# Kernel tuning notes

Hardware: AMD Instinct MI355X
Metric: run time of the kernel (lower is better)

Reference implementation:

```python
import jax, jax.numpy as jnp
import numpy as np

B, D_IN, D_OUT = 16384, 2048, 2048
BN_EPS = 1e-5


def setup_inputs() -> dict:
    key = jax.random.key(0)
    ks = jax.random.split(key, 6)
    return {
        "x": jax.random.normal(ks[0], (B, D_IN), dtype=jnp.float32),
        "base_weight": jax.random.normal(ks[1], (D_OUT, D_IN), dtype=jnp.float32) * 0.1,
        "bias": jnp.zeros((D_OUT,), dtype=jnp.float32),
        "center": jax.random.normal(ks[2], (D_IN,), dtype=jnp.float32),
        "sharpness": jnp.ones((D_IN,), dtype=jnp.float32),
        "gamma": jnp.ones((D_OUT,), dtype=jnp.float32),
        "beta": jnp.zeros((D_OUT,), dtype=jnp.float32),
        "top_k": 256,
    }


def reference(x, base_weight, bias, center, sharpness, gamma, beta, top_k):
    # fuzzy membership: sigmoid(sharpness * (x - center))  -> [B, D_in]
    mu = jax.nn.sigmoid(sharpness * (x - center))
    b, d = mu.shape

    # OWA weighted membership: keep top_k memberships, scaled by
    # normalized linspace(1.0, 0.1, top_k) weights; zeros elsewhere.
    order = jnp.argsort(-mu, axis=1)                       # descending sort indices
    sorted_vals = jnp.take_along_axis(mu, order, axis=1)
    w = jnp.linspace(1.0, 0.1, top_k, dtype=mu.dtype)
    w = w / w.sum()
    owa = jnp.zeros_like(mu).at[
        jnp.arange(b)[:, None], order[:, :top_k]
    ].set(w[None, :] * sorted_vals[:, :top_k])

    # per-sample scaled matmul: bmm(W * mu_exp, x) == (owa * x) @ W^T
    out = (owa * x) @ base_weight.T + bias                 # [B, D_out]
    out = jax.nn.relu(out)

    # BatchNorm1d in training mode: batch mean, biased variance
    mean = out.mean(axis=0)
    var = out.var(axis=0)
    y = (out - mean) * jax.lax.rsqrt(var + BN_EPS) * gamma + beta
    return (y, mu)
```

## Files before the change

### kernel.cpp

```cpp
#include <hip/hip_runtime.h>
#include <stdint.h>

#define NB 16384
#define DI 2048
#define DO 2048
#define KTOP 256
#define LIST_CAP 384
#define MT (NB / 256)

typedef __attribute__((ext_vector_type(4))) float f32x4;
typedef __attribute__((ext_vector_type(8))) short s16x8;
typedef __attribute__((ext_vector_type(8))) unsigned short u16x8;

#define OWA_C0 7.10227273e-3f
#define OWA_C1 2.50668449e-5f

__device__ __forceinline__ ushort f2bf(float f) {
  uint32_t u = __float_as_uint(f);
  uint32_t r = (u + 0x7FFFu + ((u >> 16) & 1u)) >> 16;
  return (ushort)r;
}

__device__ __forceinline__ void gld_lds16(const void* g, void* l) {
  __builtin_amdgcn_global_load_lds((__attribute__((address_space(1))) void*)g,
                                   (__attribute__((address_space(3))) void*)l,
                                   16, 0, 0);
}

__global__ __launch_bounds__(256) void k_cvt(const float* __restrict__ W,
                                             ushort* __restrict__ Wb) {
  size_t i = ((size_t)blockIdx.x * 256 + threadIdx.x) * 8;
  float4 a = *(const float4*)(W + i);
  float4 b = *(const float4*)(W + i + 4);
  u16x8 o;
  o[0] = f2bf(a.x); o[1] = f2bf(a.y); o[2] = f2bf(a.z); o[3] = f2bf(a.w);
  o[4] = f2bf(b.x); o[5] = f2bf(b.y); o[6] = f2bf(b.z); o[7] = f2bf(b.w);
  *(u16x8*)(Wb + i) = o;
}

__global__ __launch_bounds__(256) void k_topk(
    const float* __restrict__ x, const float* __restrict__ center,
    const float* __restrict__ sharp, float* __restrict__ mu_out,
    ushort* __restrict__ A) {
  __shared__ __align__(16) float w_lds[DI];
  __shared__ uint32_t histR[8 * 256];
  __shared__ uint64_t list[LIST_CAP];
  __shared__ uint32_t scal[4];

  const int t = threadIdx.x;
  const int lane = t & 63;
  const int wv = t >> 6;
  const int row = blockIdx.x;
  const int base = t * 8;

  const float* xr = x + (size_t)row * DI + base;
  float4 xa = *(const float4*)(xr);
  float4 xb = *(const float4*)(xr + 4);
  float4 ca = *(const float4*)(center + base);
  float4 cb = *(const float4*)(center + base + 4);
  float4 sa = *(const float4*)(sharp + base);
  float4 sb = *(const float4*)(sharp + base + 4);

  float xv[8] = {xa.x, xa.y, xa.z, xa.w, xb.x, xb.y, xb.z, xb.w};
  float cv[8] = {ca.x, ca.y, ca.z, ca.w, cb.x, cb.y, cb.z, cb.w};
  float sv[8] = {sa.x, sa.y, sa.z, sa.w, sb.x, sb.y, sb.z, sb.w};
  float muv[8];
  uint32_t bits[8];
#pragma unroll
  for (int e = 0; e < 8; ++e) {
    float s = sv[e] * (xv[e] - cv[e]);
    float m = 1.0f / (1.0f + __expf(-s));
    muv[e] = m;
    bits[e] = __float_as_uint(m);
  }
  if (mu_out) {
    float4 m0; m0.x = muv[0]; m0.y = muv[1]; m0.z = muv[2]; m0.w = muv[3];
    float4 m1; m1.x = muv[4]; m1.y = muv[5]; m1.z = muv[6]; m1.w = muv[7];
    *(float4*)(mu_out + (size_t)row * DI + base) = m0;
    *(float4*)(mu_out + (size_t)row * DI + base + 4) = m1;
  }
  float4 z4; z4.x = z4.y = z4.z = z4.w = 0.f;
  *(float4*)(w_lds + base) = z4;
  *(float4*)(w_lds + base + 4) = z4;

  uint32_t maskHi = 0, pfx = 0;
  uint32_t k_rem = KTOP;
  const uint32_t rep = (uint32_t)(t & 7) * 256u;
#pragma unroll 1
  for (int pass = 0; pass < 4; ++pass) {
    const int shift = 24 - pass * 8;
#pragma unroll
    for (int i = 0; i < 8; ++i) histR[t + 256 * i] = 0;
    __syncthreads();
#pragma unroll
    for (int e = 0; e < 8; ++e) {
      uint32_t bb = bits[e];
      if ((bb & maskHi) == pfx)
        atomicAdd(&histR[rep + ((bb >> shift) & 255u)], 1u);
    }
    __syncthreads();
    if (wv == 0) {
      uint32_t c0 = 0, c1 = 0, c2 = 0, c3 = 0;
#pragma unroll
      for (int r = 0; r < 8; ++r) {
        const uint32_t* h = &histR[r * 256 + lane * 4];
        c0 += h[0]; c1 += h[1]; c2 += h[2]; c3 += h[3];
      }
      uint32_t s3 = c3, s2 = c2 + s3, s1 = c1 + s2, s0 = c0 + s1;
      uint32_t Tl = s0, suf = s0;
#pragma unroll
      for (int off = 1; off < 64; off <<= 1) {
        uint32_t vsh = __shfl_down(suf, off);
        if (lane + off < 64) suf += vsh;
      }
      uint32_t above = suf - Tl;
      uint32_t SS[4] = {s0 + above, s1 + above, s2 + above, s3 + above};
      uint32_t cc[4] = {c0, c1, c2, c3};
#pragma unroll
      for (int j = 0; j < 4; ++j) {
        if (SS[j] >= k_rem && (SS[j] - cc[j]) < k_rem) {
          scal[0] = (uint32_t)(lane * 4 + j);
          scal[1] = SS[j] - cc[j];
        }
      }
    }
    __syncthreads();
    uint32_t v = scal[0], g = scal[1];
    pfx |= (v << shift);
    maskHi |= (0xFFu << shift);
    k_rem -= g;
  }
  const uint32_t tb = pfx;

  if (t == 0) scal[2] = 0;
  __syncthreads();
#pragma unroll
  for (int e = 0; e < 8; ++e) {
    if (bits[e] >= tb) {
      uint32_t pos = atomicAdd(&scal[2], 1u);
      if (pos < LIST_CAP)
        list[pos] = ((uint64_t)bits[e] << 32) |
                    (uint64_t)(uint32_t)(DI - 1 - (base + e));
    }
  }
  __syncthreads();
  int L = (int)scal[2];
  if (L > LIST_CAP) L = LIST_CAP;

  for (int sIdx = t; sIdx < L; sIdx += 256) {
    uint64_t key = list[sIdx];
    int rank = 0;
#pragma unroll 4
    for (int j = 0; j < L; ++j) rank += (int)(list[j] > key);
    if (rank < KTOP) {
      int idx = DI - 1 - (int)((uint32_t)key & 0xFFFFFFFFu);
      w_lds[idx] = OWA_C0 - OWA_C1 * (float)rank;
    }
  }
  __syncthreads();

  u16x8 ov;
#pragma unroll
  for (int e = 0; e < 8; ++e) ov[e] = f2bf(w_lds[base + e] * muv[e] * xv[e]);
  *(u16x8*)(A + (size_t)row * DI + base) = ov;
}

#define HALFS 8192

#define MFMA(a, b, c) __builtin_amdgcn_mfma_f32_16x16x32_bf16(a, b, c, 0, 0, 0)

#define STAGE_A(U, h)                                                       \
  do {                                                                      \
    ushort* sl = lA + (((((U) & 1) << 1) + (h)) * HALFS);                   \
    gld_lds16(pA0 + (size_t)((h) * 128) * DI + (size_t)(U) * 64, sl + d0);  \
    gld_lds16(pA0 + (size_t)((h) * 128 + 64) * DI + (size_t)(U) * 64,       \
              sl + d1);                                                     \
  } while (0)

#define STAGE_B(U, h)                                                       \
  do {                                                                      \
    ushort* sl = lB + (((((U) & 1) << 1) + (h)) * HALFS);                   \
    gld_lds16(pB0 + (size_t)((h) * 128) * DI + (size_t)(U) * 64, sl + d0);  \
    gld_lds16(pB0 + (size_t)((h) * 128 + 64) * DI + (size_t)(U) * 64,       \
              sl + d1);                                                     \
  } while (0)

#define RD_A(BUF, slotp, rowb)                                              \
  do {                                                                      \
    const ushort* rp_ = (slotp) + ((rowb) + fr) * 64;                       \
    BUF[0] = *(const s16x8*)(rp_ + c0);                                     \
    BUF[1] = *(const s16x8*)(rp_ + c1);                                     \
    BUF[2] = *(const s16x8*)(rp_ + 16 * 64 + c0);                           \
    BUF[3] = *(const s16x8*)(rp_ + 16 * 64 + c1);                           \
  } while (0)

#define RD_B(slotp)                                                         \
  do {                                                                      \
    _Pragma("unroll") for (int ni = 0; ni < 4; ++ni) {                      \
      breg[ni][0] = *(const s16x8*)((slotp) + ni * 1024 + boff + c0);       \
      breg[ni][1] = *(const s16x8*)((slotp) + ni * 1024 + boff + c1);       \
    }                                                                       \
  } while (0)

#define MFMA_PHASE(q, BUF)                                                  \
  do {                                                                      \
    __builtin_amdgcn_s_setprio(1);                                          \
    _Pragma("unroll") for (int ni = 0; ni < 4; ++ni) {                      \
      acc[2 * (q)][ni] = MFMA(BUF[0], breg[ni][0], acc[2 * (q)][ni]);       \
      acc[2 * (q)][ni] = MFMA(BUF[1], breg[ni][1], acc[2 * (q)][ni]);       \
      acc[2 * (q) + 1][ni] = MFMA(BUF[2], breg[ni][0], acc[2 * (q) + 1][ni]); \
      acc[2 * (q) + 1][ni] = MFMA(BUF[3], breg[ni][1], acc[2 * (q) + 1][ni]); \
    }                                                                       \
    __builtin_amdgcn_s_setprio(0);                                          \
  } while (0)

#define PHASE(q, RD_STMT, STAGE_STMT, BUF, POST_STMT, TAIL_STMT, LG)        \
  do {                                                                      \
    RD_STMT;                                                                \
    STAGE_STMT;                                                             \
    __builtin_amdgcn_s_barrier();                                           \
    asm volatile("s_waitcnt lgkmcnt(" LG ")" ::: "memory");                 \
    __builtin_amdgcn_sched_barrier(0);                                      \
    MFMA_PHASE(q, BUF);                                                     \
    POST_STMT;                                                              \
    TAIL_STMT;                                                              \
    __builtin_amdgcn_s_barrier();                                           \
  } while (0)

__global__ __launch_bounds__(512, 2) void k_gemm(
    const ushort* __restrict__ A, const ushort* __restrict__ Wb,
    const float* __restrict__ bias, float* __restrict__ outp,
    float* __restrict__ psum, float* __restrict__ psumsq) {
  __shared__ __align__(16) ushort lA[4 * HALFS];
  __shared__ __align__(16) ushort lB[4 * HALFS];

  const int t = threadIdx.x;
  const int lane = t & 63;
  const int wv = t >> 6;
  const int wm = wv >> 2;
  const int wn = wv & 3;
  const int wm32 = wm * 32;
  const int fr = lane & 15;
  const int kg = lane >> 4;
  const int s = fr & 7;

  int bid = blockIdx.x;
  int orig = (bid & 7) * 64 + (bid >> 3);
  const int nb = orig & 7;
  const int mb = orig >> 3;
  const int m0 = mb * 256;
  const int n0 = nb * 256;

  const int srow0 = t >> 3;
  const int scol = ((t & 7) ^ (srow0 & 7)) * 8;
  const ushort* pA0 = A + (size_t)(m0 + srow0) * DI + scol;
  const ushort* pB0 = Wb + (size_t)(n0 + srow0) * DI + scol;
  const int d0 = t * 8;
  const int d1 = (512 + t) * 8;

  f32x4 acc[8][4];
#pragma unroll
  for (int i = 0; i < 8; ++i)
#pragma unroll
    for (int j = 0; j < 4; ++j) acc[i][j] = (f32x4){0.f, 0.f, 0.f, 0.f};

  const int c0 = (kg ^ s) * 8;
  const int c1 = ((4 + kg) ^ s) * 8;
  const int boff = ((wn & 1) * 64 + fr) * 64;

  s16x8 breg[4][2];
  s16x8 bufA_[4], bufB_[4];

  STAGE_B(0, 0); STAGE_B(0, 1);
  STAGE_A(0, 0); STAGE_A(0, 1);
  STAGE_B(1, 0); STAGE_B(1, 1);
  asm volatile("s_waitcnt vmcnt(6)" ::: "memory");
  __builtin_amdgcn_s_barrier();
  RD_B(lB + (wn >> 1) * HALFS);
  RD_A(bufA_, lA, wm32);

#pragma unroll 1
  for (int T = 0; T < 31; ++T) {
    const ushort* lAcur = lA + ((T & 1) << 1) * HALFS;
    const ushort* lAnxt = lA + (((T + 1) & 1) << 1) * HALFS;
    const ushort* sBnxt = lB + ((((T + 1) & 1) << 1) + (wn >> 1)) * HALFS;

    PHASE(0, RD_A(bufB_, lAcur, 64 + wm32), STAGE_A(T + 1, 0), bufA_, ,
          asm volatile("s_waitcnt vmcnt(6)" ::: "memory"), "4");
    PHASE(1, RD_A(bufA_, lAcur + HALFS, wm32), STAGE_A(T + 1, 1), bufB_, , ,
          "4");
    PHASE(2, RD_A(bufB_, lAcur + HALFS, 64 + wm32),
          if (T < 30) STAGE_B(T + 2, 0), bufA_, ,
          if (T < 30) { asm volatile("s_waitcnt vmcnt(4)" ::: "memory"); }
          else { asm volatile("s_waitcnt vmcnt(2)" ::: "memory"); }, "4");
    PHASE(3, RD_A(bufA_, lAnxt, wm32), if (T < 30) STAGE_B(T + 2, 1), bufB_,
          RD_B(sBnxt), , "4");
  }
  {
    const ushort* lAcur = lA + 2 * HALFS;
    PHASE(0, RD_A(bufB_, lAcur, 64 + wm32), , bufA_, ,
          asm volatile("s_waitcnt vmcnt(0)" ::: "memory"), "4");
    PHASE(1, RD_A(bufA_, lAcur + HALFS, wm32), , bufB_, , , "4");
    PHASE(2, RD_A(bufB_, lAcur + HALFS, 64 + wm32), , bufA_, , , "4");
    PHASE(3, , , bufB_, , , "0");
  }

  __syncthreads();
  float* colsum = (float*)lA;
  float* colsq = colsum + 256;
  if (t < 256) { colsum[t] = 0.f; colsq[t] = 0.f; }
  __syncthreads();
#pragma unroll
  for (int ni = 0; ni < 4; ++ni) {
    const int n = n0 + wn * 64 + ni * 16 + fr;
    const float bv = bias[n];
    float cs = 0.f, cq = 0.f;
#pragma unroll
    for (int mi = 0; mi < 8; ++mi) {
      const int rowb = m0 + 64 * (mi >> 1) + wm32 + 16 * (mi & 1) + kg * 4;
      f32x4 v = acc[mi][ni];
#pragma unroll
      for (int r = 0; r < 4; ++r) {
        float zz = fmaxf(v[r] + bv, 0.f);
        outp[(size_t)(rowb + r) * DO + n] = zz;
        cs += zz;
        cq += zz * zz;
      }
    }
    cs += __shfl_xor(cs, 16); cq += __shfl_xor(cq, 16);
    cs += __shfl_xor(cs, 32); cq += __shfl_xor(cq, 32);
    if (kg == 0) {
      atomicAdd(&colsum[wn * 64 + ni * 16 + fr], cs);
      atomicAdd(&colsq[wn * 64 + ni * 16 + fr], cq);
    }
  }
  __syncthreads();
  if (t < 256) {
    psum[(size_t)mb * DO + n0 + t] = colsum[t];
    psumsq[(size_t)mb * DO + n0 + t] = colsq[t];
  }
}

__global__ __launch_bounds__(256) void k_bnfin(
    const float* __restrict__ psum, const float* __restrict__ psumsq,
    const float* __restrict__ gamma, const float* __restrict__ beta,
    float* __restrict__ scaleA, float* __restrict__ shiftA) {
  int n = blockIdx.x * 256 + threadIdx.x;
  float s = 0.f, q = 0.f;
  for (int r = 0; r < MT; ++r) {
    s += psum[(size_t)r * DO + n];
    q += psumsq[(size_t)r * DO + n];
  }
  float mean = s * (1.0f / (float)NB);
  float var = q * (1.0f / (float)NB) - mean * mean;
  var = fmaxf(var, 0.f);
  float rstd = rsqrtf(var + 1e-5f);
  float sc = gamma[n] * rstd;
  scaleA[n] = sc;
  shiftA[n] = beta[n] - mean * sc;
}

__global__ __launch_bounds__(256) void k_bnapply(float* __restrict__ outp,
                                                 const float* __restrict__ scaleA,
                                                 const float* __restrict__ shiftA) {
  size_t i = ((size_t)blockIdx.x * 256 + threadIdx.x) * 4;
  int n = (int)(i & (DO - 1));
  float4 v = *(float4*)(outp + i);
  float4 sc = *(const float4*)(scaleA + n);
  float4 sh = *(const float4*)(shiftA + n);
  v.x = v.x * sc.x + sh.x;
  v.y = v.y * sc.y + sh.y;
  v.z = v.z * sc.z + sh.z;
  v.w = v.w * sc.w + sh.w;
  *(float4*)(outp + i) = v;
}

__global__ __launch_bounds__(256) void k_mu(const float* __restrict__ x,
                                            const float* __restrict__ center,
                                            const float* __restrict__ sharp,
                                            float* __restrict__ mu_out) {
  const int t = threadIdx.x;
  const int row = blockIdx.x;
  const int base = t * 8;
  const float* xr = x + (size_t)row * DI + base;
  float4 xa = *(const float4*)(xr);
  float4 xb = *(const float4*)(xr + 4);
  float4 ca = *(const float4*)(center + base);
  float4 cb = *(const float4*)(center + base + 4);
  float4 sa = *(const float4*)(sharp + base);
  float4 sb = *(const float4*)(sharp + base + 4);
  float xv[8] = {xa.x, xa.y, xa.z, xa.w, xb.x, xb.y, xb.z, xb.w};
  float cv[8] = {ca.x, ca.y, ca.z, ca.w, cb.x, cb.y, cb.z, cb.w};
  float sv[8] = {sa.x, sa.y, sa.z, sa.w, sb.x, sb.y, sb.z, sb.w};
  float mu[8];
#pragma unroll
  for (int e = 0; e < 8; ++e) {
    float s = sv[e] * (xv[e] - cv[e]);
    mu[e] = 1.0f / (1.0f + __expf(-s));
  }
  float4 m0; m0.x = mu[0]; m0.y = mu[1]; m0.z = mu[2]; m0.w = mu[3];
  float4 m1; m1.x = mu[4]; m1.y = mu[5]; m1.z = mu[6]; m1.w = mu[7];
  *(float4*)(mu_out + (size_t)row * DI + base) = m0;
  *(float4*)(mu_out + (size_t)row * DI + base + 4) = m1;
}

extern "C" void kernel_launch(void* const* d_in, const int* in_sizes, int n_in,
                              void* d_out, int out_size, void* d_ws, size_t ws_size,
                              hipStream_t stream) {
  (void)in_sizes; (void)n_in; (void)out_size;
  const float* x = (const float*)d_in[0];
  const float* W = (const float*)d_in[1];
  const float* bias = (const float*)d_in[2];
  const float* center = (const float*)d_in[3];
  const float* sharp = (const float*)d_in[4];
  const float* gamma = (const float*)d_in[5];
  const float* beta = (const float*)d_in[6];

  float* outY = (float*)d_out;
  float* outMu = outY + (size_t)NB * DO;

  const size_t A_BYTES = (size_t)NB * DI * 2;
  const size_t WB_BYTES = (size_t)DO * DI * 2;
  const size_t PS_BYTES = (size_t)MT * DO * 4;
  const size_t SC_BYTES = (size_t)DO * 4;
  const size_t NEED_BIG = A_BYTES + WB_BYTES + 2 * PS_BYTES + 2 * SC_BYTES;

  char* p = (char*)d_ws;
  bool bigws = (ws_size >= NEED_BIG);
  ushort* A;
  if (bigws) { A = (ushort*)p; p += A_BYTES; }
  else       { A = (ushort*)outMu; }
  ushort* Wb = (ushort*)p; p += WB_BYTES;
  float* psum = (float*)p; p += PS_BYTES;
  float* psumsq = (float*)p; p += PS_BYTES;
  float* scaleA = (float*)p; p += SC_BYTES;
  float* shiftA = (float*)p;

  k_cvt<<<dim3((DO * DI) / (256 * 8)), dim3(256), 0, stream>>>(W, Wb);
  k_topk<<<dim3(NB), dim3(256), 0, stream>>>(x, center, sharp,
                                             bigws ? outMu : (float*)nullptr, A);
  k_gemm<<<dim3((NB / 256) * (DO / 256)), dim3(512), 0, stream>>>(A, Wb, bias, outY,
                                                                  psum, psumsq);
  k_bnfin<<<dim3(DO / 256), dim3(256), 0, stream>>>(psum, psumsq, gamma, beta,
                                                    scaleA, shiftA);
  k_bnapply<<<dim3((size_t)NB * DO / 4 / 256), dim3(256), 0, stream>>>(outY, scaleA,
                                                                       shiftA);
  if (!bigws) k_mu<<<dim3(NB), dim3(256), 0, stream>>>(x, center, sharp, outMu);
}
```

Before: 374.5 us.

## Process one row per wavefront in top-k kernel to remove block barriers

Result: slower. 413.7 us (+10.5%).

```diff
diff --git a/kernel.cpp b/kernel.cpp
--- a/kernel.cpp
+++ b/kernel.cpp
@@ -5,7 +5,7 @@
 #define DI 2048
 #define DO 2048
 #define KTOP 256
-#define LIST_CAP 384
+#define LCAP 320
 #define MT (NB / 256)
 
 typedef __attribute__((ext_vector_type(4))) float f32x4;
@@ -25,6 +25,11 @@
   __builtin_amdgcn_global_load_lds((__attribute__((address_space(1))) void*)g,
                                    (__attribute__((address_space(3))) void*)l,
                                    16, 0, 0);
+}
+
+__device__ __forceinline__ void WB() {
+  __builtin_amdgcn_wave_barrier();
+  __builtin_amdgcn_sched_barrier(0);
 }
 
 __global__ __launch_bounds__(256) void k_cvt(const float* __restrict__ W,
@@ -42,127 +47,151 @@
     const float* __restrict__ x, const float* __restrict__ center,
     const float* __restrict__ sharp, float* __restrict__ mu_out,
     ushort* __restrict__ A) {
-  __shared__ __align__(16) float w_lds[DI];
-  __shared__ uint32_t histR[8 * 256];
-  __shared__ uint64_t list[LIST_CAP];
-  __shared__ uint32_t scal[4];
-
-  const int t = threadIdx.x;
-  const int lane = t & 63;
-  const int wv = t >> 6;
-  const int row = blockIdx.x;
-  const int base = t * 8;
-
-  const float* xr = x + (size_t)row * DI + base;
-  float4 xa = *(const float4*)(xr);
-  float4 xb = *(const float4*)(xr + 4);
-  float4 ca = *(const float4*)(center + base);
-  float4 cb = *(const float4*)(center + base + 4);
-  float4 sa = *(const float4*)(sharp + base);
-  float4 sb = *(const float4*)(sharp + base + 4);
-
-  float xv[8] = {xa.x, xa.y, xa.z, xa.w, xb.x, xb.y, xb.z, xb.w};
-  float cv[8] = {ca.x, ca.y, ca.z, ca.w, cb.x, cb.y, cb.z, cb.w};
-  float sv[8] = {sa.x, sa.y, sa.z, sa.w, sb.x, sb.y, sb.z, sb.w};
-  float muv[8];
-  uint32_t bits[8];
-#pragma unroll
-  for (int e = 0; e < 8; ++e) {
-    float s = sv[e] * (xv[e] - cv[e]);
-    float m = 1.0f / (1.0f + __expf(-s));
-    muv[e] = m;
-    bits[e] = __float_as_uint(m);
-  }
-  if (mu_out) {
-    float4 m0; m0.x = muv[0]; m0.y = muv[1]; m0.z = muv[2]; m0.w = muv[3];
-    float4 m1; m1.x = muv[4]; m1.y = muv[5]; m1.z = muv[6]; m1.w = muv[7];
-    *(float4*)(mu_out + (size_t)row * DI + base) = m0;
-    *(float4*)(mu_out + (size_t)row * DI + base + 4) = m1;
-  }
-  float4 z4; z4.x = z4.y = z4.z = z4.w = 0.f;
-  *(float4*)(w_lds + base) = z4;
-  *(float4*)(w_lds + base + 4) = z4;
-
-  uint32_t maskHi = 0, pfx = 0;
-  uint32_t k_rem = KTOP;
-  const uint32_t rep = (uint32_t)(t & 7) * 256u;
+  __shared__ uint32_t hist[4][2][256];
+  __shared__ uint64_t lst[4][LCAP];
+  __shared__ ushort rnk[4][DI];
+  __shared__ uint32_t scal2[4][2];
+
+  const int lane = threadIdx.x & 63;
+  const int wv = threadIdx.x >> 6;
+  const int row = blockIdx.x * 4 + wv;
+  const int cb = lane * 32;
+
+  const float* xr = x + (size_t)row * DI + cb;
+  float p[32];
+  uint32_t bits[32];
+#pragma unroll
+  for (int c = 0; c < 8; ++c) {
+    float4 xv = *(const float4*)(xr + c * 4);
+    float4 cv = *(const float4*)(center + cb + c * 4);
+    float4 sv = *(const float4*)(sharp + cb + c * 4);
+    float m0 = 1.0f / (1.0f + __expf(-(sv.x * (xv.x - cv.x))));
+    float m1 = 1.0f / (1.0f + __expf(-(sv.y * (xv.y - cv.y))));
+    float m2 = 1.0f / (1.0f + __expf(-(sv.z * (xv.z - cv.z))));
+    float m3 = 1.0f / (1.0f + __expf(-(sv.w * (xv.w - cv.w))));
+    if (mu_out) {
+      float4 mo; mo.x = m0; mo.y = m1; mo.z = m2; mo.w = m3;
+      *(float4*)(mu_out + (size_t)row * DI + cb + c * 4) = mo;
+    }
+    bits[c * 4 + 0] = __float_as_uint(m0);
+    bits[c * 4 + 1] = __float_as_uint(m1);
+    bits[c * 4 + 2] = __float_as_uint(m2);
+    bits[c * 4 + 3] = __float_as_uint(m3);
+    p[c * 4 + 0] = m0 * xv.x;
+    p[c * 4 + 1] = m1 * xv.y;
+    p[c * 4 + 2] = m2 * xv.z;
+    p[c * 4 + 3] = m3 * xv.w;
+  }
+
+  {
+    uint32_t* hb = &hist[wv][0][0];
+    uint4 z; z.x = z.y = z.z = z.w = 0u;
+    *(uint4*)(hb + lane * 8) = z;
+    *(uint4*)(hb + lane * 8 + 4) = z;
+    uint4 ff; ff.x = ff.y = ff.z = ff.w = ~0u;
+    uint4* rb = (uint4*)&rnk[wv][0];
+    rb[lane * 4 + 0] = ff; rb[lane * 4 + 1] = ff;
+    rb[lane * 4 + 2] = ff; rb[lane * 4 + 3] = ff;
+  }
+  WB();
+
+  uint32_t maskHi = 0, pfx = 0, krem = KTOP;
+  uint32_t* h0 = &hist[wv][lane & 1][0];
 #pragma unroll 1
   for (int pass = 0; pass < 4; ++pass) {
     const int shift = 24 - pass * 8;
 #pragma unroll
-    for (int i = 0; i < 8; ++i) histR[t + 256 * i] = 0;
-    __syncthreads();
+    for (int c = 0; c < 32; ++c) {
+      if ((bits[c] & maskHi) == pfx)
+        atomicAdd(&h0[(bits[c] >> shift) & 255u], 1u);
+    }
+    WB();
+    uint4 ha = *(uint4*)&hist[wv][0][lane * 4];
+    uint4 hb4 = *(uint4*)&hist[wv][1][lane * 4];
+    uint32_t c0 = ha.x + hb4.x, c1 = ha.y + hb4.y;
+    uint32_t c2 = ha.z + hb4.z, c3 = ha.w + hb4.w;
+    uint32_t s3 = c3, s2 = c2 + s3, s1 = c1 + s2, s0 = c0 + s1;
+    uint32_t suf = s0;
+#pragma unroll
+    for (int off = 1; off < 64; off <<= 1) {
+      uint32_t v = __shfl_down(suf, off);
+      if (lane + off < 64) suf += v;
+    }
+    uint32_t above = suf - s0;
+    uint32_t SS0 = s0 + above, SS1 = s1 + above;
+    uint32_t SS2 = s2 + above, SS3 = s3 + above;
+    if (SS0 >= krem && SS0 - c0 < krem) { scal2[wv][0] = lane * 4 + 0; scal2[wv][1] = SS0 - c0; }
+    if (SS1 >= krem && SS1 - c1 < krem) { scal2[wv][0] = lane * 4 + 1; scal2[wv][1] = SS1 - c1; }
+    if (SS2 >= krem && SS2 - c2 < krem) { scal2[wv][0] = lane * 4 + 2; scal2[wv][1] = SS2 - c2; }
+    if (SS3 >= krem && SS3 - c3 < krem) { scal2[wv][0] = lane * 4 + 3; scal2[wv][1] = SS3 - c3; }
+    WB();
+    uint32_t d = scal2[wv][0], g = scal2[wv][1];
+    pfx |= (d << shift);
+    maskHi |= (0xFFu << shift);
+    krem -= g;
+    WB();
+    if (pass < 3) {
+      uint32_t* hb = &hist[wv][0][0];
+      uint4 z; z.x = z.y = z.z = z.w = 0u;
+      *(uint4*)(hb + lane * 8) = z;
+      *(uint4*)(hb + lane * 8 + 4) = z;
+      WB();
+    }
+  }
+  const uint32_t tb = pfx;
+
+  uint32_t Lc = 0;
+#pragma unroll
+  for (int c = 0; c < 32; ++c) {
+    bool pr = (bits[c] >= tb);
+    uint64_t m = __ballot(pr);
+    if (pr) {
+      uint32_t pos = Lc + (uint32_t)__popcll(m & ((1ull << lane) - 1ull));
+      if (pos < LCAP)
+        lst[wv][pos] = ((uint64_t)bits[c] << 32) |
+                       (uint64_t)(uint32_t)(DI - 1 - (cb + c));
+    }
+    Lc += (uint32_t)__popcll(m);
+  }
+  WB();
+  const int L = (Lc > LCAP) ? LCAP : (int)Lc;
+
+  uint64_t ck[5];
+#pragma unroll
+  for (int m2 = 0; m2 < 5; ++m2) {
+    int i2 = lane + 64 * m2;
+    ck[m2] = (i2 < L) ? lst[wv][i2] : ~0ull;
+  }
+  uint32_t rk[5] = {0, 0, 0, 0, 0};
+#pragma unroll 2
+  for (int j = 0; j < L; ++j) {
+    uint64_t kj = lst[wv][j];
+#pragma unroll
+    for (int m2 = 0; m2 < 5; ++m2) rk[m2] += (uint32_t)(kj > ck[m2]);
+  }
+  WB();
+#pragma unroll
+  for (int m2 = 0; m2 < 5; ++m2) {
+    int i2 = lane + 64 * m2;
+    if (i2 < L && rk[m2] < KTOP) {
+      int col = DI - 1 - (int)(uint32_t)(ck[m2] & 0xFFFFFFFFu);
+      rnk[wv][col] = (ushort)rk[m2];
+    }
+  }
+  WB();
+
+#pragma unroll
+  for (int g8 = 0; g8 < 4; ++g8) {
+    u16x8 rv = *(u16x8*)&rnk[wv][cb + g8 * 8];
+    u16x8 ov;
 #pragma unroll
     for (int e = 0; e < 8; ++e) {
-      uint32_t bb = bits[e];
-      if ((bb & maskHi) == pfx)
-        atomicAdd(&histR[rep + ((bb >> shift) & 255u)], 1u);
-    }
-    __syncthreads();
-    if (wv == 0) {
-      uint32_t c0 = 0, c1 = 0, c2 = 0, c3 = 0;
-#pragma unroll
-      for (int r = 0; r < 8; ++r) {
-        const uint32_t* h = &histR[r * 256 + lane * 4];
-        c0 += h[0]; c1 += h[1]; c2 += h[2]; c3 += h[3];
-      }
-      uint32_t s3 = c3, s2 = c2 + s3, s1 = c1 + s2, s0 = c0 + s1;
-      uint32_t Tl = s0, suf = s0;
-#pragma unroll
-      for (int off = 1; off < 64; off <<= 1) {
-        uint32_t vsh = __shfl_down(suf, off);
-        if (lane + off < 64) suf += vsh;
-      }
-      uint32_t above = suf - Tl;
-      uint32_t SS[4] = {s0 + above, s1 + above, s2 + above, s3 + above};
-      uint32_t cc[4] = {c0, c1, c2, c3};
-#pragma unroll
-      for (int j = 0; j < 4; ++j) {
-        if (SS[j] >= k_rem && (SS[j] - cc[j]) < k_rem) {
-          scal[0] = (uint32_t)(lane * 4 + j);
-          scal[1] = SS[j] - cc[j];
-        }
-      }
-    }
-    __syncthreads();
-    uint32_t v = scal[0], g = scal[1];
-    pfx |= (v << shift);
-    maskHi |= (0xFFu << shift);
-    k_rem -= g;
-  }
-  const uint32_t tb = pfx;
-
-  if (t == 0) scal[2] = 0;
-  __syncthreads();
-#pragma unroll
-  for (int e = 0; e < 8; ++e) {
-    if (bits[e] >= tb) {
-      uint32_t pos = atomicAdd(&scal[2], 1u);
-      if (pos < LIST_CAP)
-        list[pos] = ((uint64_t)bits[e] << 32) |
-                    (uint64_t)(uint32_t)(DI - 1 - (base + e));
-    }
-  }
-  __syncthreads();
-  int L = (int)scal[2];
-  if (L > LIST_CAP) L = LIST_CAP;
-
-  for (int sIdx = t; sIdx < L; sIdx += 256) {
-    uint64_t key = list[sIdx];
-    int rank = 0;
-#pragma unroll 4
-    for (int j = 0; j < L; ++j) rank += (int)(list[j] > key);
-    if (rank < KTOP) {
-      int idx = DI - 1 - (int)((uint32_t)key & 0xFFFFFFFFu);
-      w_lds[idx] = OWA_C0 - OWA_C1 * (float)rank;
-    }
-  }
-  __syncthreads();
-
-  u16x8 ov;
-#pragma unroll
-  for (int e = 0; e < 8; ++e) ov[e] = f2bf(w_lds[base + e] * muv[e] * xv[e]);
-  *(u16x8*)(A + (size_t)row * DI + base) = ov;
+      uint32_t rr = (uint32_t)(ushort)rv[e];
+      float w = (rr < KTOP) ? (OWA_C0 - OWA_C1 * (float)rr) : 0.f;
+      ov[e] = f2bf(w * p[g8 * 8 + e]);
+    }
+    *(u16x8*)(A + (size_t)row * DI + cb + g8 * 8) = ov;
+  }
 }
 
 #define HALFS 8192
@@ -437,8 +466,8 @@
   float* shiftA = (float*)p;
 
   k_cvt<<<dim3((DO * DI) / (256 * 8)), dim3(256), 0, stream>>>(W, Wb);
-  k_topk<<<dim3(NB), dim3(256), 0, stream>>>(x, center, sharp,
-                                             bigws ? outMu : (float*)nullptr, A);
+  k_topk<<<dim3(NB / 4), dim3(256), 0, stream>>>(x, center, sharp,
+                                                 bigws ? outMu : (float*)nullptr, A);
   k_gemm<<<dim3((NB / 256) * (DO / 256)), dim3(512), 0, stream>>>(A, Wb, bias, outY,
                                                                   psum, psumsq);
   k_bnfin<<<dim3(DO / 256), dim3(256), 0, stream>>>(psum, psumsq, gamma, beta,
```

## Shorten radix top-k select to two passes with wave-aggregated list append

Applied to the files above, without the earlier changes.

New measurement: 371.5 us. About the same (-0.8%).

```diff
diff --git a/kernel.cpp b/kernel.cpp
--- a/kernel.cpp
+++ b/kernel.cpp
@@ -45,7 +45,7 @@
   __shared__ __align__(16) float w_lds[DI];
   __shared__ uint32_t histR[8 * 256];
   __shared__ uint64_t list[LIST_CAP];
-  __shared__ uint32_t scal[4];
+  __shared__ uint32_t scal[8];
 
   const int t = threadIdx.x;
   const int lane = t & 63;
@@ -82,22 +82,26 @@
   float4 z4; z4.x = z4.y = z4.z = z4.w = 0.f;
   *(float4*)(w_lds + base) = z4;
   *(float4*)(w_lds + base + 4) = z4;
-
-  uint32_t maskHi = 0, pfx = 0;
-  uint32_t k_rem = KTOP;
+  if (t == 0) scal[2] = 0;
+
   const uint32_t rep = (uint32_t)(t & 7) * 256u;
-#pragma unroll 1
-  for (int pass = 0; pass < 4; ++pass) {
-    const int shift = 24 - pass * 8;
+
+  uint32_t nhi = 0;
+#pragma unroll
+  for (int e = 0; e < 8; ++e) nhi += (bits[e] >> 24) == 0x3Fu;
+#pragma unroll
+  for (int off = 1; off < 64; off <<= 1) nhi += __shfl_xor(nhi, off);
+  if (lane == 0) scal[4 + wv] = nhi;
+  __syncthreads();
+  const uint32_t c_hi = scal[4] + scal[5] + scal[6] + scal[7];
+
+  uint32_t maskHi = 0xFF000000u, pfx = 0x3F000000u, krem = KTOP;
+  if (c_hi < KTOP) {
 #pragma unroll
     for (int i = 0; i < 8; ++i) histR[t + 256 * i] = 0;
     __syncthreads();
 #pragma unroll
-    for (int e = 0; e < 8; ++e) {
-      uint32_t bb = bits[e];
-      if ((bb & maskHi) == pfx)
-        atomicAdd(&histR[rep + ((bb >> shift) & 255u)], 1u);
-    }
+    for (int e = 0; e < 8; ++e) atomicAdd(&histR[rep + (bits[e] >> 24)], 1u);
     __syncthreads();
     if (wv == 0) {
       uint32_t c0 = 0, c1 = 0, c2 = 0, c3 = 0;
@@ -110,37 +114,78 @@
       uint32_t Tl = s0, suf = s0;
 #pragma unroll
       for (int off = 1; off < 64; off <<= 1) {
-        uint32_t vsh = __shfl_down(suf, off);
-        if (lane + off < 64) suf += vsh;
+        uint32_t v = __shfl_down(suf, off);
+        if (lane + off < 64) suf += v;
       }
       uint32_t above = suf - Tl;
       uint32_t SS[4] = {s0 + above, s1 + above, s2 + above, s3 + above};
       uint32_t cc[4] = {c0, c1, c2, c3};
 #pragma unroll
       for (int j = 0; j < 4; ++j) {
-        if (SS[j] >= k_rem && (SS[j] - cc[j]) < k_rem) {
+        if (SS[j] >= KTOP && (SS[j] - cc[j]) < KTOP) {
           scal[0] = (uint32_t)(lane * 4 + j);
           scal[1] = SS[j] - cc[j];
         }
       }
     }
     __syncthreads();
-    uint32_t v = scal[0], g = scal[1];
-    pfx |= (v << shift);
-    maskHi |= (0xFFu << shift);
-    k_rem -= g;
-  }
-  const uint32_t tb = pfx;
-
-  if (t == 0) scal[2] = 0;
+    pfx = scal[0] << 24;
+    krem = KTOP - scal[1];
+  }
+
+#pragma unroll
+  for (int i = 0; i < 8; ++i) histR[t + 256 * i] = 0;
   __syncthreads();
 #pragma unroll
   for (int e = 0; e < 8; ++e) {
-    if (bits[e] >= tb) {
-      uint32_t pos = atomicAdd(&scal[2], 1u);
-      if (pos < LIST_CAP)
-        list[pos] = ((uint64_t)bits[e] << 32) |
-                    (uint64_t)(uint32_t)(DI - 1 - (base + e));
+    if ((bits[e] & maskHi) == pfx)
+      atomicAdd(&histR[rep + ((bits[e] >> 16) & 255u)], 1u);
+  }
+  __syncthreads();
+  if (wv == 0) {
+    uint32_t c0 = 0, c1 = 0, c2 = 0, c3 = 0;
+#pragma unroll
+    for (int r = 0; r < 8; ++r) {
+      const uint32_t* h = &histR[r * 256 + lane * 4];
+      c0 += h[0]; c1 += h[1]; c2 += h[2]; c3 += h[3];
+    }
+    uint32_t s3 = c3, s2 = c2 + s3, s1 = c1 + s2, s0 = c0 + s1;
+    uint32_t Tl = s0, suf = s0;
+#pragma unroll
+    for (int off = 1; off < 64; off <<= 1) {
+      uint32_t v = __shfl_down(suf, off);
+      if (lane + off < 64) suf += v;
+    }
+    uint32_t above = suf - Tl;
+    uint32_t SS[4] = {s0 + above, s1 + above, s2 + above, s3 + above};
+    uint32_t cc[4] = {c0, c1, c2, c3};
+#pragma unroll
+    for (int j = 0; j < 4; ++j) {
+      if (SS[j] >= krem && (SS[j] - cc[j]) < krem) {
+        scal[0] = (uint32_t)(lane * 4 + j);
+        scal[1] = SS[j] - cc[j];
+      }
+    }
+  }
+  __syncthreads();
+  const uint32_t tb = pfx | (scal[0] << 16);
+
+  const uint64_t lmask_lt = (1ull << lane) - 1ull;
+#pragma unroll
+  for (int e = 0; e < 8; ++e) {
+    bool pr = (bits[e] >= tb);
+    uint64_t m = __ballot(pr);
+    uint32_t cnt = (uint32_t)__popcll(m);
+    if (cnt) {
+      uint32_t wbase = 0;
+      if (lane == 0) wbase = atomicAdd(&scal[2], cnt);
+      wbase = __shfl(wbase, 0);
+      if (pr) {
+        uint32_t pos = wbase + (uint32_t)__popcll(m & lmask_lt);
+        if (pos < LIST_CAP)
+          list[pos] = ((uint64_t)bits[e] << 32) |
+                      (uint64_t)(uint32_t)(DI - 1 - (base + e));
+      }
     }
   }
   __syncthreads();
```
